# Kernel tuning notes

Hardware: AMD Instinct MI355X
Metric: run time of the kernel (lower is better)

Reference implementation:

```python
import jax, jax.numpy as jnp
import numpy as np

# module hyper-params (from NLSearch __init__ defaults)
K = 7        # top-k neighbors
PS = 7       # patch size
WS = 8       # search window (ws x ws candidates)
NHEADS = 1
STRIDE0 = 4  # query grid stride
STRIDE1 = 1  # candidate stride within window


def _reflect(i, n):
    # reflect (mirror) out-of-range indices into [0, n)
    i = jnp.where(i < 0, -i, i)
    return jnp.where(i >= n, 2 * (n - 1) - i, i)


def setup_inputs() -> dict:
    key = jax.random.key(0)
    k0, k1 = jax.random.split(key)
    vid0 = jax.random.normal(k0, (1, 3, 32, 256, 256), dtype=jnp.float32)
    vid1 = jax.random.normal(k1, (1, 3, 32, 256, 256), dtype=jnp.float32)
    return {"vid0": vid0, "vid1": vid1}


def _nl_search(vid0, vid1):
    B, T, C, H, W = vid0.shape
    HD = NHEADS
    c = C // HD
    v0 = vid0.reshape(B, T, HD, c, H, W)
    v1 = vid1.reshape(B, T, HD, c, H, W)
    nH = (H - 1) // STRIDE0 + 1
    nW = (W - 1) // STRIDE0 + 1
    qh = jnp.arange(nH) * STRIDE0  # query centers
    qw = jnp.arange(nW) * STRIDE0
    poff = jnp.arange(PS) - PS // 2  # centered patch offsets

    def patches(v, hc, wc):
        # gather reflect-bounded ps x ps patches centered at (hc, wc)
        hi = _reflect(hc[:, None] + poff[None, :], H)  # [nH, PS]
        wi = _reflect(wc[:, None] + poff[None, :], W)  # [nW, PS]
        p = v[:, :, :, :, hi]          # [B,T,HD,c,nH,PS,W]
        p = p[:, :, :, :, :, :, wi]    # [B,T,HD,c,nH,PS,nW,PS]
        return p

    p0 = patches(v0, qh, qw)  # query patches, reused across all shifts
    woff = (jnp.arange(WS) - WS // 2) * STRIDE1
    shifts = jnp.stack(jnp.meshgrid(woff, woff, indexing='ij'), -1).reshape(-1, 2)  # [WS*WS,2]

    def body(carry, s):
        def step(s_):
            p1 = patches(v1, qh + s_[0], qw + s_[1])
            # patch inner product ('prod' search distance)
            return jnp.einsum('bthcnivj,bthcnivj->bthnv', p0, p1)
        return carry, jax.checkpoint(step)(s)

    _, dists = jax.lax.scan(body, 0, shifts)   # [L,B,T,HD,nH,nW]
    dists = jnp.moveaxis(dists, 0, -1)         # [B,T,HD,nH,nW,L]

    # anchor_self: force the self (zero-shift) candidate to rank first,
    # but return its true distance (bump only used for ordering)
    self_idx = (WS // 2) * WS + (WS // 2)
    adj = dists.at[..., self_idx].add(jnp.asarray(1e30, dists.dtype))
    _, top_idx = jax.lax.top_k(adj, K)                       # [B,T,HD,nH,nW,K]
    top_d = jnp.take_along_axis(dists, top_idx, axis=-1)     # [B,T,HD,nH,nW,K]

    # decode flat shift index -> absolute (t,h,w) neighbor coordinates
    dh = (top_idx // WS - WS // 2) * STRIDE1
    dw = (top_idx % WS - WS // 2) * STRIDE1
    hh = _reflect(qh[None, None, None, :, None, None] + dh, H)
    ww = _reflect(qw[None, None, None, None, :, None] + dw, W)
    tt = jnp.broadcast_to(jnp.arange(T)[None, :, None, None, None, None], hh.shape)
    inds = jnp.stack([tt, hh, ww], -1)  # [B,T,HD,nH,nW,K,3]

    Q = T * nH * nW
    dists_out = jnp.transpose(top_d, (0, 2, 1, 3, 4, 5)).reshape(B, HD, Q, K)
    inds_out = jnp.transpose(inds, (0, 2, 1, 3, 4, 5, 6)).reshape(B, HD, Q, K, 3)
    return dists_out, inds_out


def reference(vid0, vid1):
    return _nl_search(vid0, vid1)
```

## Files before the change

### kernel.cpp

```cpp
#include <hip/hip_runtime.h>

#define TT 3
#define CCH 32
#define HH 256
#define WW 256
#define KK 7
#define NQ 64
#define QPB 16
#define V1W 76
#define V1R 14
#define V1N (V1R*V1W)
#define V1P 1088
#define V0W 72
#define V0N (7*V0W)
#define V0P 512
#define CHC 8
#define NCHUNK 4

__device__ __forceinline__ int refl(int i, int n) {
    i = i < 0 ? -i : i;
    return i >= n ? 2*(n-1) - i : i;
}

__device__ __forceinline__ void gload_lds(const float* g, float* l) {
    __builtin_amdgcn_global_load_lds(
        (const __attribute__((address_space(1))) unsigned int*)g,
        (__attribute__((address_space(3))) unsigned int*)l, 4, 0, 0);
}

#define XL(I, XA, XB) { const float4* xp = (const float4*)(xbase + (I)*V0W); \
                        XA = xp[0]; XB = xp[1]; }
#define YPREF(RR, N0,N1,N2,N3) { \
    const float4* yp = (const float4*)(ybase + (4*shh + (RR)) * V1W); \
    N0 = yp[0]; N1 = yp[1]; N2 = yp[2]; N3 = yp[3]; }
#define YMAT(C0,C1,C2,C3) const float y[16] = { \
    C0.x,C0.y,C0.z,C0.w, C1.x,C1.y,C1.z,C1.w, \
    C2.x,C2.y,C2.z,C2.w, C3.x,C3.y,C3.z,C3.w };
#define FMAROW(AIDX, XA, XB) { \
    _Pragma("unroll") for (int sw = 0; sw < 8; ++sw) { \
        acc[AIDX][sw] += XA.x*y[sw+0]; acc[AIDX][sw] += XA.y*y[sw+1]; \
        acc[AIDX][sw] += XA.z*y[sw+2]; acc[AIDX][sw] += XA.w*y[sw+3]; \
        acc[AIDX][sw] += XB.x*y[sw+4]; acc[AIDX][sw] += XB.y*y[sw+5]; \
        acc[AIDX][sw] += XB.z*y[sw+6]; } }

__global__ __launch_bounds__(256)
void nls_kernel(const float* __restrict__ vid0, const float* __restrict__ vid1,
                float* __restrict__ out) {
    __shared__ float v1s[CHC * V1P];
    __shared__ float v0s[CHC * V0P];

    const int bx  = blockIdx.x;
    const int t   = bx >> 8;
    const int rem = bx & 255;
    const int qy  = rem >> 2;
    const int q0  = (rem & 3) * QPB;
    const int qh  = qy * 4;
    const int w0  = 4*q0 - 7;

    const int tid   = threadIdx.x;
    const int qwi   = tid & 15;
    const int c01   = (tid >> 4) & 3;
    const int c2    = (tid >> 6) & 1;
    const int shh   = tid >> 7;
    const int clane = c01 + 4*c2;

    int off1[5];
#pragma unroll
    for (int k = 0; k < 5; ++k) {
        int idx = tid + 256*k;
        if (idx < V1N) {
            int r = idx / V1W, wi = idx - r*V1W;
            off1[k] = refl(qh + r - 7, HH) * WW + refl(w0 + wi, WW);
        } else off1[k] = 0;
    }
    int off0[2];
#pragma unroll
    for (int k = 0; k < 2; ++k) {
        int idx = tid + 256*k;
        if (idx < V0N) {
            int r = idx / V0W, wi = idx - r*V0W;
            off0[k] = refl(qh + r - 3, HH) * WW + refl(w0 + wi, WW);
        } else off0[k] = 0;
    }

    float acc[4][8];
#pragma unroll
    for (int a = 0; a < 4; ++a)
#pragma unroll
        for (int b = 0; b < 8; ++b) acc[a][b] = 0.f;

    const float* g0t = vid0 + (size_t)t * (CCH*HH*WW);
    const float* g1t = vid1 + (size_t)t * (CCH*HH*WW);

#pragma unroll 1
    for (int s = 0; s < NCHUNK; ++s) {
        __syncthreads();
#pragma unroll
        for (int ch = 0; ch < CHC; ++ch) {
            const float* p1 = g1t + (size_t)(CHC*s + ch) * (HH*WW);
            float* lb = &v1s[ch*V1P + (tid & ~63)];
#pragma unroll
            for (int k = 0; k < 4; ++k)
                gload_lds(p1 + off1[k], lb + 256*k);
            if (tid < V1N - 1024)
                gload_lds(p1 + off1[4], &v1s[ch*V1P + 1024 + (tid & ~63)]);
        }
#pragma unroll
        for (int ch = 0; ch < CHC; ++ch) {
            const float* p0 = g0t + (size_t)(CHC*s + ch) * (HH*WW);
            float* lb0 = &v0s[ch*V0P + (tid & ~63)];
            gload_lds(p0 + off0[0], lb0);
            if (tid < V0N - 256)
                gload_lds(p0 + off0[1], lb0 + 256);
        }
        __syncthreads();

        const float* xbase = &v0s[clane*V0P + 4*qwi + 4];
        const float* ybase = &v1s[clane*V1P + 4*qwi];
        float4 X0a,X0b,X1a,X1b,X2a,X2b,X3a,X3b,X4a,X4b,X5a,X5b,X6a,X6b;
        float4 Ya0,Ya1,Ya2,Ya3, Yb0,Yb1,Yb2,Yb3;
        XL(0, X0a,X0b)
        YPREF(0, Ya0,Ya1,Ya2,Ya3)
        { YPREF(1, Yb0,Yb1,Yb2,Yb3) XL(1, X1a,X1b) YMAT(Ya0,Ya1,Ya2,Ya3)
          FMAROW(0, X0a,X0b) }
        { YPREF(2, Ya0,Ya1,Ya2,Ya3) XL(2, X2a,X2b) YMAT(Yb0,Yb1,Yb2,Yb3)
          FMAROW(0, X1a,X1b) FMAROW(1, X0a,X0b) }
        { YPREF(3, Yb0,Yb1,Yb2,Yb3) XL(3, X3a,X3b) YMAT(Ya0,Ya1,Ya2,Ya3)
          FMAROW(0, X2a,X2b) FMAROW(1, X1a,X1b) FMAROW(2, X0a,X0b) }
        { YPREF(4, Ya0,Ya1,Ya2,Ya3) XL(4, X4a,X4b) YMAT(Yb0,Yb1,Yb2,Yb3)
          FMAROW(0, X3a,X3b) FMAROW(1, X2a,X2b) FMAROW(2, X1a,X1b) FMAROW(3, X0a,X0b) }
        { YPREF(5, Yb0,Yb1,Yb2,Yb3) XL(5, X5a,X5b) YMAT(Ya0,Ya1,Ya2,Ya3)
          FMAROW(0, X4a,X4b) FMAROW(1, X3a,X3b) FMAROW(2, X2a,X2b) FMAROW(3, X1a,X1b) }
        { YPREF(6, Ya0,Ya1,Ya2,Ya3) XL(6, X6a,X6b) YMAT(Yb0,Yb1,Yb2,Yb3)
          FMAROW(0, X5a,X5b) FMAROW(1, X4a,X4b) FMAROW(2, X3a,X3b) FMAROW(3, X2a,X2b) }
        { YPREF(7, Yb0,Yb1,Yb2,Yb3) YMAT(Ya0,Ya1,Ya2,Ya3)
          FMAROW(0, X6a,X6b) FMAROW(1, X5a,X5b) FMAROW(2, X4a,X4b) FMAROW(3, X3a,X3b) }
        { YPREF(8, Ya0,Ya1,Ya2,Ya3) YMAT(Yb0,Yb1,Yb2,Yb3)
          FMAROW(1, X6a,X6b) FMAROW(2, X5a,X5b) FMAROW(3, X4a,X4b) }
        { YPREF(9, Yb0,Yb1,Yb2,Yb3) YMAT(Ya0,Ya1,Ya2,Ya3)
          FMAROW(2, X6a,X6b) FMAROW(3, X5a,X5b) }
        { YMAT(Yb0,Yb1,Yb2,Yb3)
          FMAROW(3, X6a,X6b) }
    }

#pragma unroll
    for (int m = 16; m <= 32; m <<= 1)
#pragma unroll
        for (int a = 0; a < 4; ++a)
#pragma unroll
            for (int b = 0; b < 8; ++b)
                acc[a][b] += __shfl_xor(acc[a][b], m, 64);

    __syncthreads();
    float* dlds = v1s;
    if (c01 == 0) {
#pragma unroll
        for (int a = 0; a < 4; ++a) {
            float* dp = &dlds[c2*1024 + qwi*64 + (shh*4 + a)*8];
            *(float4*)(dp)     = make_float4(acc[a][0], acc[a][1], acc[a][2], acc[a][3]);
            *(float4*)(dp + 4) = make_float4(acc[a][4], acc[a][5], acc[a][6], acc[a][7]);
        }
    }
    __syncthreads();

    {
        const int q16 = tid >> 4;
        const int l16 = tid & 15;
        const float* d0 = &dlds[q16 * 64];
        const float* d1 = d0 + 1024;
        const int j0 = l16 * 4;
        float cv[4];
#pragma unroll
        for (int jj = 0; jj < 4; ++jj) {
            float v = d0[j0 + jj] + d1[j0 + jj];
            if (j0 + jj == 36) v += 1e30f;
            cv[jj] = v;
        }
        unsigned mask = 0;
        const int qxx = q0 + q16;
        const int q   = (t*NQ + qy)*NQ + qxx;
        float* od = out + q*KK;
        float* oi = out + (size_t)TT*NQ*NQ*KK + (size_t)q*KK*3;
        for (int k = 0; k < KK; ++k) {
            float best = -3.4e38f; int bi = 1 << 30;
#pragma unroll
            for (int jj = 0; jj < 4; ++jj)
                if (!(mask & (1u << jj)) && cv[jj] > best) { best = cv[jj]; bi = j0 + jj; }
#pragma unroll
            for (int m = 1; m <= 8; m <<= 1) {
                float ob = __shfl_xor(best, m, 64);
                int  obi = __shfl_xor(bi,  m, 64);
                if (ob > best || (ob == best && obi < bi)) { best = ob; bi = obi; }
            }
            if ((bi >> 2) == l16) mask |= 1u << (bi & 3);
            if (l16 == 0) {
                od[k] = d0[bi] + d1[bi];
                int dh = (bi >> 3) - 4;
                int dw = (bi & 7) - 4;
                oi[k*3 + 0] = (float)t;
                oi[k*3 + 1] = (float)refl(qh + dh, HH);
                oi[k*3 + 2] = (float)refl(qxx*4 + dw, WW);
            }
        }
    }
}

extern "C" void kernel_launch(void* const* d_in, const int* in_sizes, int n_in,
                              void* d_out, int out_size, void* d_ws, size_t ws_size,
                              hipStream_t stream) {
    (void)in_sizes; (void)n_in; (void)d_ws; (void)ws_size; (void)out_size;
    const float* vid0 = (const float*)d_in[0];
    const float* vid1 = (const float*)d_in[1];
    float* out = (float*)d_out;
    nls_kernel<<<dim3(TT * NQ * (NQ / QPB)), dim3(256), 0, stream>>>(vid0, vid1, out);
}
```

Baseline: 126.1 us.

## Halve queries per block and remap threads to 8 channel lanes, 2 shift rows

Each block now handles 8 query columns instead of 16, doubling the grid. Threads are remapped so 8 channel lanes each handle 2 shift rows, replacing 4 rows split across two channel groups. The cross-half LDS reduction and the padded LDS strides go away, and the top-k selection now spans 32 lanes. Smaller tiles mean more halo is reloaded per query and fewer FMAs per LDS load, traded for more blocks and lower register use.

New measurement: 135.9 us. 7.8% more time.

```diff
diff --git a/kernel.cpp b/kernel.cpp
--- a/kernel.cpp
+++ b/kernel.cpp
@@ -6,14 +6,13 @@
 #define WW 256
 #define KK 7
 #define NQ 64
-#define QPB 16
-#define V1W 76
+#define QPB 8
+#define V1W 48
 #define V1R 14
 #define V1N (V1R*V1W)
-#define V1P 1088
-#define V0W 72
-#define V0N (7*V0W)
-#define V0P 512
+#define V0W 40
+#define V0R 7
+#define V0N (V0R*V0W)
 #define CHC 8
 #define NCHUNK 4
 
@@ -28,45 +27,42 @@
         (__attribute__((address_space(3))) unsigned int*)l, 4, 0, 0);
 }
 
-#define XL(I, XA, XB) { const float4* xp = (const float4*)(xbase + (I)*V0W); \
-                        XA = xp[0]; XB = xp[1]; }
-#define YPREF(RR, N0,N1,N2,N3) { \
-    const float4* yp = (const float4*)(ybase + (4*shh + (RR)) * V1W); \
-    N0 = yp[0]; N1 = yp[1]; N2 = yp[2]; N3 = yp[3]; }
+#define XLD(PI, XA, XB) { const float4* xp = (const float4*)(xb + (PI)*V0W); \
+                          XA = xp[0]; XB = xp[1]; }
+#define YLD(RR, N0,N1,N2,N3) { const float4* yp = (const float4*)(yb + (RR)*V1W); \
+                               N0 = yp[0]; N1 = yp[1]; N2 = yp[2]; N3 = yp[3]; }
 #define YMAT(C0,C1,C2,C3) const float y[16] = { \
     C0.x,C0.y,C0.z,C0.w, C1.x,C1.y,C1.z,C1.w, \
     C2.x,C2.y,C2.z,C2.w, C3.x,C3.y,C3.z,C3.w };
-#define FMAROW(AIDX, XA, XB) { \
-    _Pragma("unroll") for (int sw = 0; sw < 8; ++sw) { \
-        acc[AIDX][sw] += XA.x*y[sw+0]; acc[AIDX][sw] += XA.y*y[sw+1]; \
-        acc[AIDX][sw] += XA.z*y[sw+2]; acc[AIDX][sw] += XA.w*y[sw+3]; \
-        acc[AIDX][sw] += XB.x*y[sw+4]; acc[AIDX][sw] += XB.y*y[sw+5]; \
-        acc[AIDX][sw] += XB.z*y[sw+6]; } }
+#define FROW(L, XA, XB) { _Pragma("unroll") for (int sw = 0; sw < 8; ++sw) { \
+    acc[L][sw] += XA.x*y[sw+0]; acc[L][sw] += XA.y*y[sw+1]; \
+    acc[L][sw] += XA.z*y[sw+2]; acc[L][sw] += XA.w*y[sw+3]; \
+    acc[L][sw] += XB.x*y[sw+4]; acc[L][sw] += XB.y*y[sw+5]; \
+    acc[L][sw] += XB.z*y[sw+6]; } }
 
 __global__ __launch_bounds__(256)
 void nls_kernel(const float* __restrict__ vid0, const float* __restrict__ vid1,
                 float* __restrict__ out) {
-    __shared__ float v1s[CHC * V1P];
-    __shared__ float v0s[CHC * V0P];
+    __shared__ float v1s[CHC * V1N];
+    __shared__ float v0s[CHC * V0N];
 
     const int bx  = blockIdx.x;
-    const int t   = bx >> 8;
-    const int rem = bx & 255;
-    const int qy  = rem >> 2;
-    const int q0  = (rem & 3) * QPB;
+    const int t   = bx >> 9;
+    const int rem = bx & 511;
+    const int qy  = rem >> 3;
+    const int q0  = (rem & 7) * QPB;
     const int qh  = qy * 4;
     const int w0  = 4*q0 - 7;
+    const int w0x = 4*q0 - 3;
 
     const int tid   = threadIdx.x;
-    const int qwi   = tid & 15;
-    const int c01   = (tid >> 4) & 3;
-    const int c2    = (tid >> 6) & 1;
-    const int shh   = tid >> 7;
-    const int clane = c01 + 4*c2;
-
-    int off1[5];
-#pragma unroll
-    for (int k = 0; k < 5; ++k) {
+    const int qwi   = tid & 7;
+    const int clane = (tid >> 3) & 7;
+    const int shq   = tid >> 6;
+
+    int off1[3];
+#pragma unroll
+    for (int k = 0; k < 3; ++k) {
         int idx = tid + 256*k;
         if (idx < V1N) {
             int r = idx / V1W, wi = idx - r*V1W;
@@ -79,15 +75,15 @@
         int idx = tid + 256*k;
         if (idx < V0N) {
             int r = idx / V0W, wi = idx - r*V0W;
-            off0[k] = refl(qh + r - 3, HH) * WW + refl(w0 + wi, WW);
+            off0[k] = refl(qh + r - 3, HH) * WW + refl(w0x + wi, WW);
         } else off0[k] = 0;
     }
 
-    float acc[4][8];
-#pragma unroll
-    for (int a = 0; a < 4; ++a)
-#pragma unroll
-        for (int b = 0; b < 8; ++b) acc[a][b] = 0.f;
+    float acc[2][8];
+#pragma unroll
+    for (int l = 0; l < 2; ++l)
+#pragma unroll
+        for (int b = 0; b < 8; ++b) acc[l][b] = 0.f;
 
     const float* g0t = vid0 + (size_t)t * (CCH*HH*WW);
     const float* g1t = vid1 + (size_t)t * (CCH*HH*WW);
@@ -98,103 +94,97 @@
 #pragma unroll
         for (int ch = 0; ch < CHC; ++ch) {
             const float* p1 = g1t + (size_t)(CHC*s + ch) * (HH*WW);
-            float* lb = &v1s[ch*V1P + (tid & ~63)];
-#pragma unroll
-            for (int k = 0; k < 4; ++k)
-                gload_lds(p1 + off1[k], lb + 256*k);
-            if (tid < V1N - 1024)
-                gload_lds(p1 + off1[4], &v1s[ch*V1P + 1024 + (tid & ~63)]);
+            float* lb = &v1s[ch*V1N + (tid & ~63)];
+            gload_lds(p1 + off1[0], lb);
+            gload_lds(p1 + off1[1], lb + 256);
+            if (tid < V1N - 512)
+                gload_lds(p1 + off1[2], lb + 512);
         }
 #pragma unroll
         for (int ch = 0; ch < CHC; ++ch) {
             const float* p0 = g0t + (size_t)(CHC*s + ch) * (HH*WW);
-            float* lb0 = &v0s[ch*V0P + (tid & ~63)];
+            float* lb0 = &v0s[ch*V0N + (tid & ~63)];
             gload_lds(p0 + off0[0], lb0);
             if (tid < V0N - 256)
                 gload_lds(p0 + off0[1], lb0 + 256);
         }
         __syncthreads();
 
-        const float* xbase = &v0s[clane*V0P + 4*qwi + 4];
-        const float* ybase = &v1s[clane*V1P + 4*qwi];
-        float4 X0a,X0b,X1a,X1b,X2a,X2b,X3a,X3b,X4a,X4b,X5a,X5b,X6a,X6b;
+        const float* xb = &v0s[clane*V0N + 4*qwi];
+        const float* yb = &v1s[clane*V1N + 2*shq*V1W + 4*qwi];
+        float4 Xa0,Xa1, Xb0,Xb1, Xc0,Xc1;
         float4 Ya0,Ya1,Ya2,Ya3, Yb0,Yb1,Yb2,Yb3;
-        XL(0, X0a,X0b)
-        YPREF(0, Ya0,Ya1,Ya2,Ya3)
-        { YPREF(1, Yb0,Yb1,Yb2,Yb3) XL(1, X1a,X1b) YMAT(Ya0,Ya1,Ya2,Ya3)
-          FMAROW(0, X0a,X0b) }
-        { YPREF(2, Ya0,Ya1,Ya2,Ya3) XL(2, X2a,X2b) YMAT(Yb0,Yb1,Yb2,Yb3)
-          FMAROW(0, X1a,X1b) FMAROW(1, X0a,X0b) }
-        { YPREF(3, Yb0,Yb1,Yb2,Yb3) XL(3, X3a,X3b) YMAT(Ya0,Ya1,Ya2,Ya3)
-          FMAROW(0, X2a,X2b) FMAROW(1, X1a,X1b) FMAROW(2, X0a,X0b) }
-        { YPREF(4, Ya0,Ya1,Ya2,Ya3) XL(4, X4a,X4b) YMAT(Yb0,Yb1,Yb2,Yb3)
-          FMAROW(0, X3a,X3b) FMAROW(1, X2a,X2b) FMAROW(2, X1a,X1b) FMAROW(3, X0a,X0b) }
-        { YPREF(5, Yb0,Yb1,Yb2,Yb3) XL(5, X5a,X5b) YMAT(Ya0,Ya1,Ya2,Ya3)
-          FMAROW(0, X4a,X4b) FMAROW(1, X3a,X3b) FMAROW(2, X2a,X2b) FMAROW(3, X1a,X1b) }
-        { YPREF(6, Ya0,Ya1,Ya2,Ya3) XL(6, X6a,X6b) YMAT(Yb0,Yb1,Yb2,Yb3)
-          FMAROW(0, X5a,X5b) FMAROW(1, X4a,X4b) FMAROW(2, X3a,X3b) FMAROW(3, X2a,X2b) }
-        { YPREF(7, Yb0,Yb1,Yb2,Yb3) YMAT(Ya0,Ya1,Ya2,Ya3)
-          FMAROW(0, X6a,X6b) FMAROW(1, X5a,X5b) FMAROW(2, X4a,X4b) FMAROW(3, X3a,X3b) }
-        { YPREF(8, Ya0,Ya1,Ya2,Ya3) YMAT(Yb0,Yb1,Yb2,Yb3)
-          FMAROW(1, X6a,X6b) FMAROW(2, X5a,X5b) FMAROW(3, X4a,X4b) }
-        { YPREF(9, Yb0,Yb1,Yb2,Yb3) YMAT(Ya0,Ya1,Ya2,Ya3)
-          FMAROW(2, X6a,X6b) FMAROW(3, X5a,X5b) }
+        XLD(0, Xa0,Xa1)
+        YLD(0, Ya0,Ya1,Ya2,Ya3)
+        { YLD(1, Yb0,Yb1,Yb2,Yb3) XLD(1, Xb0,Xb1) YMAT(Ya0,Ya1,Ya2,Ya3)
+          FROW(0, Xa0,Xa1) }
+        { YLD(2, Ya0,Ya1,Ya2,Ya3) XLD(2, Xc0,Xc1) YMAT(Yb0,Yb1,Yb2,Yb3)
+          FROW(0, Xb0,Xb1) FROW(1, Xa0,Xa1) }
+        { YLD(3, Yb0,Yb1,Yb2,Yb3) XLD(3, Xa0,Xa1) YMAT(Ya0,Ya1,Ya2,Ya3)
+          FROW(0, Xc0,Xc1) FROW(1, Xb0,Xb1) }
+        { YLD(4, Ya0,Ya1,Ya2,Ya3) XLD(4, Xb0,Xb1) YMAT(Yb0,Yb1,Yb2,Yb3)
+          FROW(0, Xa0,Xa1) FROW(1, Xc0,Xc1) }
+        { YLD(5, Yb0,Yb1,Yb2,Yb3) XLD(5, Xc0,Xc1) YMAT(Ya0,Ya1,Ya2,Ya3)
+          FROW(0, Xb0,Xb1) FROW(1, Xa0,Xa1) }
+        { YLD(6, Ya0,Ya1,Ya2,Ya3) XLD(6, Xa0,Xa1) YMAT(Yb0,Yb1,Yb2,Yb3)
+          FROW(0, Xc0,Xc1) FROW(1, Xb0,Xb1) }
+        { YLD(7, Yb0,Yb1,Yb2,Yb3) YMAT(Ya0,Ya1,Ya2,Ya3)
+          FROW(0, Xa0,Xa1) FROW(1, Xc0,Xc1) }
         { YMAT(Yb0,Yb1,Yb2,Yb3)
-          FMAROW(3, X6a,X6b) }
-    }
-
-#pragma unroll
-    for (int m = 16; m <= 32; m <<= 1)
-#pragma unroll
-        for (int a = 0; a < 4; ++a)
+          FROW(1, Xa0,Xa1) }
+    }
+
+#pragma unroll
+    for (int m = 8; m <= 32; m <<= 1)
+#pragma unroll
+        for (int l = 0; l < 2; ++l)
 #pragma unroll
             for (int b = 0; b < 8; ++b)
-                acc[a][b] += __shfl_xor(acc[a][b], m, 64);
+                acc[l][b] += __shfl_xor(acc[l][b], m, 64);
 
     __syncthreads();
     float* dlds = v1s;
-    if (c01 == 0) {
-#pragma unroll
-        for (int a = 0; a < 4; ++a) {
-            float* dp = &dlds[c2*1024 + qwi*64 + (shh*4 + a)*8];
-            *(float4*)(dp)     = make_float4(acc[a][0], acc[a][1], acc[a][2], acc[a][3]);
-            *(float4*)(dp + 4) = make_float4(acc[a][4], acc[a][5], acc[a][6], acc[a][7]);
+    if (clane == 0) {
+#pragma unroll
+        for (int l = 0; l < 2; ++l) {
+            float* dp = &dlds[qwi*64 + (2*shq + l)*8];
+            *(float4*)(dp)     = make_float4(acc[l][0], acc[l][1], acc[l][2], acc[l][3]);
+            *(float4*)(dp + 4) = make_float4(acc[l][4], acc[l][5], acc[l][6], acc[l][7]);
         }
     }
     __syncthreads();
 
     {
-        const int q16 = tid >> 4;
-        const int l16 = tid & 15;
-        const float* d0 = &dlds[q16 * 64];
-        const float* d1 = d0 + 1024;
-        const int j0 = l16 * 4;
-        float cv[4];
-#pragma unroll
-        for (int jj = 0; jj < 4; ++jj) {
-            float v = d0[j0 + jj] + d1[j0 + jj];
+        const int q8  = tid >> 5;
+        const int l32 = tid & 31;
+        const float* d = &dlds[q8 * 64];
+        const int j0 = l32 * 2;
+        float cv[2];
+#pragma unroll
+        for (int jj = 0; jj < 2; ++jj) {
+            float v = d[j0 + jj];
             if (j0 + jj == 36) v += 1e30f;
             cv[jj] = v;
         }
         unsigned mask = 0;
-        const int qxx = q0 + q16;
+        const int qxx = q0 + q8;
         const int q   = (t*NQ + qy)*NQ + qxx;
         float* od = out + q*KK;
         float* oi = out + (size_t)TT*NQ*NQ*KK + (size_t)q*KK*3;
         for (int k = 0; k < KK; ++k) {
             float best = -3.4e38f; int bi = 1 << 30;
 #pragma unroll
-            for (int jj = 0; jj < 4; ++jj)
+            for (int jj = 0; jj < 2; ++jj)
                 if (!(mask & (1u << jj)) && cv[jj] > best) { best = cv[jj]; bi = j0 + jj; }
 #pragma unroll
-            for (int m = 1; m <= 8; m <<= 1) {
+            for (int m = 1; m <= 16; m <<= 1) {
                 float ob = __shfl_xor(best, m, 64);
                 int  obi = __shfl_xor(bi,  m, 64);
                 if (ob > best || (ob == best && obi < bi)) { best = ob; bi = obi; }
             }
-            if ((bi >> 2) == l16) mask |= 1u << (bi & 3);
-            if (l16 == 0) {
-                od[k] = d0[bi] + d1[bi];
+            if ((bi >> 1) == l32) mask |= 1u << (bi & 1);
+            if (l32 == 0) {
+                od[k] = d[bi];
                 int dh = (bi >> 3) - 4;
                 int dw = (bi & 7) - 4;
                 oi[k*3 + 0] = (float)t;
```
